# Kernel tuning notes

Measured on AMD Instinct MI355X. Metric: run time of the kernel, lower is better.

Reference implementation:

```python
import jax, jax.numpy as jnp
import numpy as np
import math

NUM_HEADS = 16
VEC_SIZE = 1024
HEAD_DIM = VEC_SIZE // NUM_HEADS


def setup_inputs() -> dict:
    key = jax.random.key(0)
    k1, k2, k3, k4, k5 = jax.random.split(key, 5)
    B, S, D = 2, 2048, VEC_SIZE
    x = jax.random.normal(k1, (B, S, D), dtype=jnp.float32)
    # Linear params, torch-style: y = x @ W.T + b
    s1 = 1.0 / math.sqrt(D)
    W_qkv = jax.random.uniform(k2, (3 * D, D), minval=-s1, maxval=s1, dtype=jnp.float32)
    b_qkv = jax.random.uniform(k3, (3 * D,), minval=-s1, maxval=s1, dtype=jnp.float32)
    W_out = jax.random.uniform(k4, (D, D), minval=-s1, maxval=s1, dtype=jnp.float32)
    b_out = jax.random.uniform(k5, (D,), minval=-s1, maxval=s1, dtype=jnp.float32)
    return {"x": x, "W_qkv": W_qkv, "b_qkv": b_qkv, "W_out": W_out, "b_out": b_out}


def reference(x, W_qkv, b_qkv, W_out, b_out):
    B, S, D = x.shape
    H, Hd = NUM_HEADS, HEAD_DIM
    qkv = x @ W_qkv.T + b_qkv                      # [B,S,3D]
    q, k, v = jnp.split(qkv, 3, axis=-1)
    # [B,S,H,Hd] -> [B,H,S,Hd]
    q = q.reshape(B, S, H, Hd).transpose(0, 2, 1, 3)
    k = k.reshape(B, S, H, Hd).transpose(0, 2, 1, 3)
    v = v.reshape(B, S, H, Hd).transpose(0, 2, 1, 3)
    weight = jnp.einsum('bhqd,bhkd->bhqk', q, k)   # [B,H,S,S]
    causal = jnp.triu(jnp.ones((S, S), dtype=bool), k=1)
    weight = jnp.where(causal, -jnp.inf, weight)
    weight = weight / jnp.sqrt(jnp.asarray(Hd, dtype=weight.dtype))
    weight = jax.nn.softmax(weight, axis=-1)
    out = jnp.einsum('bhqk,bhkd->bhqd', weight, v)  # [B,H,S,Hd]
    out = out.transpose(0, 2, 1, 3).reshape(B, S, D)
    return out @ W_out.T + b_out
```

## Files before the change

### kernel.cpp

```cpp
#include <hip/hip_runtime.h>
#include <hip/hip_bf16.h>

typedef __attribute__((ext_vector_type(8))) short short8;
typedef __attribute__((ext_vector_type(4))) short s4v;
typedef __attribute__((ext_vector_type(4))) float floatx4;

__device__ inline floatx4 mfma_bf16(short8 a, short8 b, floatx4 c) {
  return __builtin_amdgcn_mfma_f32_16x16x32_bf16(a, b, c, 0, 0, 0);
}
__device__ inline float exp2_fast(float x) { return __builtin_amdgcn_exp2f(x); }

__device__ inline short bf16s(float f) {
  __hip_bfloat16 h = __float2bfloat16(f);
  return *reinterpret_cast<short*>(&h);
}
__device__ inline float sbf16(short s) {
  return __bfloat162float(*reinterpret_cast<__hip_bfloat16*>(&s));
}

__device__ inline void gld16(__hip_bfloat16* lds, const __hip_bfloat16* g) {
  __builtin_amdgcn_global_load_lds(
      (const __attribute__((address_space(1))) void*)g,
      (__attribute__((address_space(3))) void*)lds, 16, 0, 0);
}

__global__ __launch_bounds__(256) void cvt_all(
    const float* __restrict__ x, const float* __restrict__ wqkv,
    const float* __restrict__ wout, __hip_bfloat16* __restrict__ xb,
    __hip_bfloat16* __restrict__ wqkvb, __hip_bfloat16* __restrict__ wob) {
  const int n1 = 4194304, n2 = 3145728;
  int i = (blockIdx.x * 256 + threadIdx.x) * 8;
  const float* src;
  __hip_bfloat16* dst;
  int off;
  if (i < n1) { src = x; dst = xb; off = i; }
  else if (i < n1 + n2) { src = wqkv; dst = wqkvb; off = i - n1; }
  else { src = wout; dst = wob; off = i - n1 - n2; }
  float4 a = *reinterpret_cast<const float4*>(src + off);
  float4 b = *reinterpret_cast<const float4*>(src + off + 4);
  __hip_bfloat16 t[8];
  t[0] = __float2bfloat16(a.x); t[1] = __float2bfloat16(a.y);
  t[2] = __float2bfloat16(a.z); t[3] = __float2bfloat16(a.w);
  t[4] = __float2bfloat16(b.x); t[5] = __float2bfloat16(b.y);
  t[6] = __float2bfloat16(b.z); t[7] = __float2bfloat16(b.w);
  *reinterpret_cast<short8*>(dst + off) = *reinterpret_cast<short8*>(t);
}

template<int TN, bool OUT_BF16>
__global__ __launch_bounds__(256) void gemm_bt(
    const __hip_bfloat16* __restrict__ A, const __hip_bfloat16* __restrict__ Bt,
    const float* __restrict__ bias, void* __restrict__ Cout,
    int M, int N, int K) {
  __shared__ __align__(16) __hip_bfloat16 As[128 * 64];
  __shared__ __align__(16) __hip_bfloat16 Bs[TN * 64];
  const int tid = threadIdx.x;
  const int wave = tid >> 6, lane = tid & 63, quad = lane >> 4, l15 = lane & 15;
  const int wm = (wave >> 1) * 64, wn = (wave & 1) * (TN / 2);
  const int m0 = blockIdx.y * 128, n0 = blockIdx.x * TN;
  const int NC = TN / 32;

  floatx4 acc[4][NC];
  for (int r = 0; r < 4; ++r)
    for (int c = 0; c < NC; ++c) acc[r][c] = (floatx4){0.f, 0.f, 0.f, 0.f};

  for (int k0 = 0; k0 < K; k0 += 64) {
    __syncthreads();
    for (int it = 0; it < 4; ++it) {
      int idx = it * 256 + tid;
      int row = idx >> 3, col = ((idx & 7) ^ (row & 7)) * 8;
      gld16(&As[idx * 8], A + (size_t)(m0 + row) * K + k0 + col);
    }
    for (int it = 0; it < TN * 64 / 2048; ++it) {
      int idx = it * 256 + tid;
      int row = idx >> 3, col = ((idx & 7) ^ (row & 7)) * 8;
      gld16(&Bs[idx * 8], Bt + (size_t)(n0 + row) * K + k0 + col);
    }
    __syncthreads();
    for (int ks = 0; ks < 2; ++ks) {
      short8 af[4], bf[NC];
      for (int r = 0; r < 4; ++r) {
        int row = wm + r * 16 + l15;
        af[r] = *reinterpret_cast<const short8*>(
            &As[row * 64 + (((ks * 4 + quad) ^ (l15 & 7)) * 8)]);
      }
      for (int c = 0; c < NC; ++c) {
        int row = wn + c * 16 + l15;
        bf[c] = *reinterpret_cast<const short8*>(
            &Bs[row * 64 + (((ks * 4 + quad) ^ (l15 & 7)) * 8)]);
      }
      for (int r = 0; r < 4; ++r)
        for (int c = 0; c < NC; ++c)
          acc[r][c] = mfma_bf16(af[r], bf[c], acc[r][c]);
    }
  }

  for (int c = 0; c < NC; ++c) {
    int gn = n0 + wn + c * 16 + l15;
    float bv = bias[gn];
    for (int r = 0; r < 4; ++r)
      for (int rg = 0; rg < 4; ++rg) {
        int gm = m0 + wm + r * 16 + quad * 4 + rg;
        float v = acc[r][c][rg] + bv;
        if (OUT_BF16)
          ((__hip_bfloat16*)Cout)[(size_t)gm * N + gn] = __float2bfloat16(v);
        else
          ((float*)Cout)[(size_t)gm * N + gn] = v;
      }
  }
}

__global__ __launch_bounds__(256, 4) void flash_attn(
    const __hip_bfloat16* __restrict__ qkv, __hip_bfloat16* __restrict__ out) {
  const int S = 2048, QKV = 3072;
  const int bx = blockIdx.x;
  const int g = (blockIdx.y >> 3) + 2 * blockIdx.z;
  int qt;
  if (g == 0)      qt = bx;
  else if (g == 1) qt = 31 - bx;
  else if (g == 2) qt = (bx + 8) & 31;
  else             qt = (23 - bx) & 31;
  const int h = blockIdx.y, b = blockIdx.z;
  const int q0 = qt * 64;
  __shared__ __align__(16) short Ps[2][64 * 64];
  const int tid = threadIdx.x;
  const int wave = tid >> 6, lane = tid & 63, quad = lane >> 4, l15 = lane & 15;
  const int rx = l15 & 7;
  const __hip_bfloat16* base = qkv + (size_t)b * S * QKV;
  const float c2 = 0.18033688011112042f;
  const floatx4 zero4 = {0.f, 0.f, 0.f, 0.f};
  const int krow = 16 * wave + l15;

  const __hip_bfloat16* kbase = base + 1024 + h * 64;
  const __hip_bfloat16* vbase = base + 2048 + h * 64;

  for (int it = 0; it < 2; ++it) {
    int v = tid + it * 256;
    int row = v >> 3, cb = v & 7;
    int colp = (cb ^ (row & 7)) * 8;
    short8 qv = *reinterpret_cast<const short8*>(
        base + (size_t)(q0 + row) * QKV + h * 64 + cb * 8);
    short qs[8];
    for (int e = 0; e < 8; ++e) qs[e] = bf16s(sbf16(qv[e]) * c2);
    *reinterpret_cast<short8*>(&Ps[1][row * 64 + colp]) = *reinterpret_cast<short8*>(qs);
  }
  short8 kA0 = *reinterpret_cast<const short8*>(
      kbase + (size_t)krow * QKV + quad * 8);
  short8 kA1 = *reinterpret_cast<const short8*>(
      kbase + (size_t)krow * QKV + 32 + quad * 8);
  __syncthreads();

  short8 aq[4][2];
  for (int t4 = 0; t4 < 4; ++t4)
    for (int s = 0; s < 2; ++s)
      aq[t4][s] = *reinterpret_cast<const short8*>(
          &Ps[1][(t4 * 16 + l15) * 64 + (((s * 4 + quad) ^ rx) * 8)]);

  floatx4 o_acc[4];
  for (int m = 0; m < 4; ++m) o_acc[m] = zero4;
  float lsum4[4] = {0.f, 0.f, 0.f, 0.f};
  short8 vA0, vA1;

  for (int j = 0; j <= qt; ++j) {
    const int cj = j & 1, pj = cj ^ 1;

    short8 kB0, kB1, vB0, vB1;
    if (j < qt) {
      const __hip_bfloat16* kp = kbase + (size_t)((j + 1) * 64 + krow) * QKV;
      kB0 = *reinterpret_cast<const short8*>(kp + quad * 8);
      kB1 = *reinterpret_cast<const short8*>(kp + 32 + quad * 8);
    }
    {
      const __hip_bfloat16* vp = vbase + (size_t)(j * 64 + quad * 8) * QKV + krow;
      for (int i = 0; i < 8; ++i) {
        vB0[i] = *reinterpret_cast<const short*>(vp + (size_t)i * QKV);
        vB1[i] = *reinterpret_cast<const short*>(vp + (size_t)(32 + i) * QKV);
      }
    }

    if (j > 0) {
      for (int s = 0; s < 2; ++s) {
        short8 bv = s ? vA1 : vA0;
        for (int m = 0; m < 4; ++m) {
          short8 ap = *reinterpret_cast<const short8*>(
              &Ps[pj][(m * 16 + l15) * 64 + (((4 * s + quad) ^ rx) * 8)]);
          o_acc[m] = mfma_bf16(ap, bv, o_acc[m]);
        }
      }
    }

    floatx4 sc[4];
    for (int t4 = 0; t4 < 4; ++t4) {
      sc[t4] = mfma_bf16(kA0, aq[t4][0], zero4);
      sc[t4] = mfma_bf16(kA1, aq[t4][1], sc[t4]);
    }
    if (j == qt) {
      int kloc = 16 * wave + quad * 4;
      for (int t4 = 0; t4 < 4; ++t4)
        for (int rg = 0; rg < 4; ++rg)
          if (kloc + rg > t4 * 16 + l15) sc[t4][rg] = -1e30f;
    }

    const int pcol = ((2 * wave + (quad >> 1)) ^ rx) * 8 + (quad & 1) * 4;
    for (int t4 = 0; t4 < 4; ++t4) {
      short pp[4];
      for (int rg = 0; rg < 4; ++rg) {
        float p = exp2_fast(sc[t4][rg]);
        lsum4[t4] += p;
        pp[rg] = bf16s(p);
      }
      *reinterpret_cast<s4v*>(&Ps[cj][(t4 * 16 + l15) * 64 + pcol]) =
          *reinterpret_cast<s4v*>(pp);
    }

    kA0 = kB0; kA1 = kB1; vA0 = vB0; vA1 = vB1;
    __syncthreads();
  }

  const int pq = qt & 1;
  for (int s = 0; s < 2; ++s) {
    short8 bv = s ? vA1 : vA0;
    for (int m = 0; m < 4; ++m) {
      short8 ap = *reinterpret_cast<const short8*>(
          &Ps[pq][(m * 16 + l15) * 64 + (((4 * s + quad) ^ rx) * 8)]);
      o_acc[m] = mfma_bf16(ap, bv, o_acc[m]);
    }
  }
  for (int t4 = 0; t4 < 4; ++t4) {
    lsum4[t4] += __shfl_xor(lsum4[t4], 16);
    lsum4[t4] += __shfl_xor(lsum4[t4], 32);
  }
  float* Lf = (float*)&Ps[pq ^ 1][0];
  if (quad == 0)
    for (int t4 = 0; t4 < 4; ++t4)
      Lf[wave * 64 + t4 * 16 + l15] = lsum4[t4];
  __syncthreads();
  if (tid < 64)
    Lf[256 + tid] = 1.0f / (Lf[tid] + Lf[64 + tid] + Lf[128 + tid] + Lf[192 + tid]);
  __syncthreads();

  const int dcol = h * 64 + krow;
  for (int m = 0; m < 4; ++m)
    for (int rg = 0; rg < 4; ++rg) {
      int q = m * 16 + quad * 4 + rg;
      out[(size_t)(b * S + q0 + q) * 1024 + dcol] =
          __float2bfloat16(o_acc[m][rg] * Lf[256 + q]);
    }
}

extern "C" void kernel_launch(void* const* d_in, const int* in_sizes, int n_in,
                              void* d_out, int out_size, void* d_ws, size_t ws_size,
                              hipStream_t stream) {
  const float* x    = (const float*)d_in[0];
  const float* Wqkv = (const float*)d_in[1];
  const float* bqkv = (const float*)d_in[2];
  const float* Wout = (const float*)d_in[3];
  const float* bout = (const float*)d_in[4];
  float* out = (float*)d_out;

  const int BS = 2 * 2048;
  const int D = 1024;
  char* ws = (char*)d_ws;
  __hip_bfloat16* xb    = (__hip_bfloat16*)(ws);
  __hip_bfloat16* wqkvb = (__hip_bfloat16*)(ws + (size_t)8  * 1048576);
  __hip_bfloat16* wob   = (__hip_bfloat16*)(ws + (size_t)14 * 1048576);
  __hip_bfloat16* qkvb  = (__hip_bfloat16*)(ws + (size_t)16 * 1048576);
  __hip_bfloat16* attnb = (__hip_bfloat16*)(ws + (size_t)40 * 1048576);

  cvt_all<<<4096, 256, 0, stream>>>(x, Wqkv, Wout, xb, wqkvb, wob);

  gemm_bt<128, true><<<dim3(3072 / 128, BS / 128), 256, 0, stream>>>(
      xb, wqkvb, bqkv, qkvb, BS, 3 * D, D);

  flash_attn<<<dim3(32, 16, 2), 256, 0, stream>>>(qkvb, attnb);

  gemm_bt<64, false><<<dim3(1024 / 64, BS / 128), 256, 0, stream>>>(
      attnb, wob, bout, out, BS, D, D);
}
```

Before: 181.3 us.

## Add 256x256-tile 8-wave GEMM with phased LDS pipelining for QKV projection

Adds a new QKV projection GEMM kernel that uses 256x256 output tiles with 512 threads. The tile is split into four 128x128 quadrant phases, each staging the next k-slice of one half-tile through direct global-to-LDS loads while MFMAs run on the current buffer. It also remaps block IDs across XCDs and raises wave priority around the MFMA bursts. The larger tile aims to increase data reuse and overlap loads with compute, at the cost of more registers, more LDS, and fewer blocks (192) to fill the GPU.

```diff
diff --git a/kernel.cpp b/kernel.cpp
--- a/kernel.cpp
+++ b/kernel.cpp
@@ -109,6 +109,126 @@
   }
 }
 
+__device__ inline void stage_half(__hip_bfloat16* lds, const __hip_bfloat16* g,
+                                  int K, int tid) {
+#pragma unroll
+  for (int it = 0; it < 2; ++it) {
+    int idx = it * 512 + tid;
+    int row = idx >> 3, col = ((idx & 7) ^ (row & 7)) * 8;
+    gld16(lds + idx * 8, g + (size_t)row * K + col);
+  }
+}
+
+#define PHASE(MH, NH, STAGE_STMT, VM)                                          \
+  do {                                                                         \
+    if (NH == 0) {                                                             \
+      _Pragma("unroll") for (int mf = 0; mf < 4; ++mf) {                       \
+        int rh = wm * 64 + mf * 16 + l15;                                      \
+        _Pragma("unroll") for (int ks = 0; ks < 2; ++ks)                       \
+            af[mf][ks] = *reinterpret_cast<const short8*>(                     \
+                &SA[cb][MH][rh * 64 + (((ks * 4 + quad) ^ (rh & 7)) * 8)]);    \
+      }                                                                        \
+    }                                                                          \
+    _Pragma("unroll") for (int nf = 0; nf < 2; ++nf) {                         \
+      int rh = wn * 32 + nf * 16 + l15;                                        \
+      _Pragma("unroll") for (int ks = 0; ks < 2; ++ks)                         \
+          bf[nf][ks] = *reinterpret_cast<const short8*>(                       \
+              &SB[cb][NH][rh * 64 + (((ks * 4 + quad) ^ (rh & 7)) * 8)]);      \
+    }                                                                          \
+    STAGE_STMT;                                                                \
+    __builtin_amdgcn_s_barrier();                                              \
+    __builtin_amdgcn_s_setprio(1);                                             \
+    _Pragma("unroll") for (int mf = 0; mf < 4; ++mf)                           \
+        _Pragma("unroll") for (int nf = 0; nf < 2; ++nf) {                     \
+      acc[MH][NH][mf][nf] = mfma_bf16(af[mf][0], bf[nf][0], acc[MH][NH][mf][nf]); \
+      acc[MH][NH][mf][nf] = mfma_bf16(af[mf][1], bf[nf][1], acc[MH][NH][mf][nf]); \
+    }                                                                          \
+    __builtin_amdgcn_s_setprio(0);                                             \
+    asm volatile("s_waitcnt vmcnt(" #VM ")" ::: "memory");                     \
+    __builtin_amdgcn_s_barrier();                                              \
+  } while (0)
+
+template<bool OUT_BF16>
+__global__ __launch_bounds__(512, 2) void gemm_256(
+    const __hip_bfloat16* __restrict__ A, const __hip_bfloat16* __restrict__ Bt,
+    const float* __restrict__ bias, void* __restrict__ Cout,
+    int M, int N, int K) {
+  __shared__ __align__(16) __hip_bfloat16 SA[2][2][128 * 64];
+  __shared__ __align__(16) __hip_bfloat16 SB[2][2][128 * 64];
+  const int tid = threadIdx.x;
+  const int lane = tid & 63, quad = (lane >> 4), l15 = lane & 15;
+  const int wave = tid >> 6;
+  const int wm = wave >> 2, wn = wave & 3;
+
+  const int nbx = gridDim.x;
+  int bid = blockIdx.y * nbx + blockIdx.x;
+  const int nwg = nbx * gridDim.y;
+  if ((nwg & 7) == 0) bid = (bid & 7) * (nwg >> 3) + (bid >> 3);
+  const int bx = bid % nbx, by = bid / nbx;
+  const int m0 = by * 256, n0 = bx * 256;
+
+  const __hip_bfloat16* Abase = A + (size_t)m0 * K;
+  const __hip_bfloat16* Bbase = Bt + (size_t)n0 * K;
+  const int NT = K >> 6;
+
+  floatx4 acc[2][2][4][2];
+#pragma unroll
+  for (int a = 0; a < 2; ++a)
+#pragma unroll
+    for (int b = 0; b < 2; ++b)
+#pragma unroll
+      for (int c = 0; c < 4; ++c)
+#pragma unroll
+        for (int d = 0; d < 2; ++d) acc[a][b][c][d] = (floatx4){0.f, 0.f, 0.f, 0.f};
+
+  short8 af[4][2];
+  short8 bf[2][2];
+
+  stage_half(&SA[0][0][0], Abase, K, tid);
+  stage_half(&SB[0][0][0], Bbase, K, tid);
+  stage_half(&SB[0][1][0], Bbase + (size_t)128 * K, K, tid);
+  stage_half(&SA[0][1][0], Abase + (size_t)128 * K, K, tid);
+  asm volatile("s_waitcnt vmcnt(4)" ::: "memory");
+  __builtin_amdgcn_s_barrier();
+
+  for (int t = 0; t < NT - 1; ++t) {
+    const int cb = t & 1, nb = cb ^ 1;
+    const int k1 = (t + 1) * 64;
+    PHASE(0, 0, stage_half(&SA[nb][0][0], Abase + k1, K, tid), 4);
+    PHASE(0, 1, stage_half(&SB[nb][0][0], Bbase + k1, K, tid), 4);
+    PHASE(1, 0, stage_half(&SB[nb][1][0], Bbase + (size_t)128 * K + k1, K, tid), 4);
+    PHASE(1, 1, stage_half(&SA[nb][1][0], Abase + (size_t)128 * K + k1, K, tid), 4);
+  }
+  {
+    const int cb = (NT - 1) & 1;
+    PHASE(0, 0, (void)0, 2);
+    PHASE(0, 1, (void)0, 0);
+    PHASE(1, 0, (void)0, 0);
+    PHASE(1, 1, (void)0, 0);
+  }
+
+#pragma unroll
+  for (int nh = 0; nh < 2; ++nh)
+#pragma unroll
+    for (int nf = 0; nf < 2; ++nf) {
+      int gn = n0 + nh * 128 + wn * 32 + nf * 16 + l15;
+      float bv = bias[gn];
+#pragma unroll
+      for (int mh = 0; mh < 2; ++mh)
+#pragma unroll
+        for (int mf = 0; mf < 4; ++mf)
+#pragma unroll
+          for (int rg = 0; rg < 4; ++rg) {
+            int gm = m0 + mh * 128 + wm * 64 + mf * 16 + quad * 4 + rg;
+            float v = acc[mh][nh][mf][nf][rg] + bv;
+            if (OUT_BF16)
+              ((__hip_bfloat16*)Cout)[(size_t)gm * N + gn] = __float2bfloat16(v);
+            else
+              ((float*)Cout)[(size_t)gm * N + gn] = v;
+          }
+    }
+}
+
 __global__ __launch_bounds__(256, 4) void flash_attn(
     const __hip_bfloat16* __restrict__ qkv, __hip_bfloat16* __restrict__ out) {
   const int S = 2048, QKV = 3072;
@@ -268,7 +388,7 @@
 
   cvt_all<<<4096, 256, 0, stream>>>(x, Wqkv, Wout, xb, wqkvb, wob);
 
-  gemm_bt<128, true><<<dim3(3072 / 128, BS / 128), 256, 0, stream>>>(
+  gemm_256<true><<<dim3(3072 / 256, BS / 256), 512, 0, stream>>>(
       xb, wqkvb, bqkv, qkvb, BS, 3 * D, D);
 
   flash_attn<<<dim3(32, 16, 2), 256, 0, stream>>>(qkvb, attnb);
```

Result: faster. 177.3 us (-2.2%).
